# Kernel tuning notes

Measured on AMD Instinct MI355X. Metric: run time of the kernel, lower is better.

The kernel has to match this reference:

```python
import jax, jax.numpy as jnp
import numpy as np

E, NH, NL, NP = 256, 8, 4, 4
D = E // NH
SPATIAL_SHAPES = np.array([[100, 134], [50, 67], [25, 34], [13, 17]], dtype=np.int64)
B = 2


def setup_inputs() -> dict:
    key = jax.random.key(0)
    ks = jax.random.split(key, 12)
    Lin = int((SPATIAL_SHAPES[:, 0] * SPATIAL_SHAPES[:, 1]).sum())
    Lq = Lin
    s = 0.02
    return {
        'query': jax.random.normal(ks[0], (Lq, B, E), jnp.float32),
        'value': jax.random.normal(ks[1], (Lin, B, E), jnp.float32),
        'reference_points': jax.random.uniform(ks[2], (B, Lq, NL, 2), jnp.float32),
        'spatial_shapes': SPATIAL_SHAPES,
        'W_value': jax.random.normal(ks[3], (E, E), jnp.float32) * s,
        'b_value': jnp.zeros((E,), jnp.float32),
        'W_offset': jax.random.normal(ks[4], (E, NH * NL * NP * 2), jnp.float32) * s,
        'b_offset': jax.random.normal(ks[5], (NH * NL * NP * 2,), jnp.float32) * 0.5,
        'W_attn': jax.random.normal(ks[6], (E, NH * NL * NP), jnp.float32) * s,
        'b_attn': jnp.zeros((NH * NL * NP,), jnp.float32),
        'W_out': jax.random.normal(ks[7], (E, E), jnp.float32) * s,
        'b_out': jnp.zeros((E,), jnp.float32),
    }


def _ms_deform_attn(value, spatial_shapes, sampling_locations, attention_weights):
    # value: (B, Lin, NH, D); sampling_locations: (B, Lq, NH, NL, NP, 2) in [0,1]
    # attention_weights: (B, Lq, NH, NL, NP)
    b, _, nh, d = value.shape
    lq = sampling_locations.shape[1]
    npnt = sampling_locations.shape[4]
    shapes = np.asarray(spatial_shapes)
    out = jnp.zeros((b, nh, lq, d), value.dtype)
    start = 0
    for l in range(shapes.shape[0]):
        H, W = int(shapes[l, 0]), int(shapes[l, 1])
        vl = value[:, start:start + H * W].transpose(0, 2, 1, 3)  # (B, NH, H*W, D)
        loc = sampling_locations[:, :, :, l].transpose(0, 2, 1, 3, 4)  # (B, NH, Lq, P, 2)
        # grid_sample align_corners=False convention (matches CUDA kernel)
        x = loc[..., 0] * W - 0.5
        y = loc[..., 1] * H - 0.5
        x0 = jnp.floor(x)
        y0 = jnp.floor(y)
        dx = x - x0
        dy = y - y0
        x0i = x0.astype(jnp.int32)
        y0i = y0.astype(jnp.int32)
        acc = jnp.zeros((b, nh, lq, npnt, d), value.dtype)
        corners = [
            (x0i, y0i, (1.0 - dx) * (1.0 - dy)),
            (x0i + 1, y0i, dx * (1.0 - dy)),
            (x0i, y0i + 1, (1.0 - dx) * dy),
            (x0i + 1, y0i + 1, dx * dy),
        ]
        for xi, yi, w in corners:
            valid = ((xi >= 0) & (xi < W) & (yi >= 0) & (yi < H)).astype(value.dtype)
            idx = jnp.clip(yi, 0, W - 1 if False else H - 1) * 0  # placeholder removed below
            idx = jnp.clip(yi, 0, H - 1) * W + jnp.clip(xi, 0, W - 1)  # (B, NH, Lq, P)
            g = jnp.take_along_axis(vl, idx.reshape(b, nh, -1)[..., None], axis=2)
            g = g.reshape(b, nh, lq, npnt, d)
            acc = acc + g * (w * valid)[..., None]
        awl = attention_weights[:, :, :, l].transpose(0, 2, 1, 3)  # (B, NH, Lq, P)
        out = out + jnp.einsum('bhqpd,bhqp->bhqd', acc, awl)
        start += H * W
    return out.transpose(0, 2, 1, 3).reshape(b, lq, nh * d)  # (B, Lq, E)


def reference(query, value, reference_points, spatial_shapes,
              W_value, b_value, W_offset, b_offset, W_attn, b_attn, W_out, b_out):
    q = query.transpose(1, 0, 2)   # (B, Lq, E)
    v = value.transpose(1, 0, 2)   # (B, Lin, E)
    b, lq, _ = q.shape
    lin = v.shape[1]
    v = (v @ W_value + b_value).reshape(b, lin, NH, D)
    offsets = (q @ W_offset + b_offset).reshape(b, lq, NH, NL, NP, 2)
    attn = (q @ W_attn + b_attn).reshape(b, lq, NH, NL, NP)
    attn = jax.nn.softmax(attn, axis=-1)  # softmax over points (as in source)
    shapes_f = jnp.asarray(np.asarray(spatial_shapes), jnp.float32)
    offset_normalizer = jnp.stack([shapes_f[:, 1], shapes_f[:, 0]], -1)  # (NL, 2) = (w, h)
    loc = reference_points[:, :, None, :, None, :] + offsets / offset_normalizer[None, None, None, :, None, :]
    out = _ms_deform_attn(v, spatial_shapes, loc, attn)  # (B, Lq, E)
    out = out @ W_out + b_out
    return out.transpose(1, 0, 2)  # (Lq, B, E)
```

## Files before the change

kernel.cpp:

```cpp
#include <hip/hip_runtime.h>
#include <math.h>

#define LQ    17821
#define MROWS 35642
#define KD    256

typedef __attribute__((ext_vector_type(8))) short bf16x8;
typedef __attribute__((ext_vector_type(4))) float f32x4;

__device__ __forceinline__ short f2bf(float f) {
  union { float f; unsigned u; } c; c.f = f;
  unsigned u = c.u;
  return (short)((u + 0x7fffu + ((u >> 16) & 1u)) >> 16);
}
__device__ __forceinline__ float bf2f(short s) {
  union { unsigned u; float f; } c;
  c.u = ((unsigned)(unsigned short)s) << 16;
  return c.f;
}

__global__ __launch_bounds__(256) void wtrans_all(
    const float* __restrict__ Wv, const float* __restrict__ Woff,
    const float* __restrict__ Wat, const float* __restrict__ Wout,
    const float* __restrict__ boff, const float* __restrict__ bat,
    short* __restrict__ wT, float* __restrict__ fbias)
{
  int sel = blockIdx.y;
  int idx = blockIdx.x * 256 + threadIdx.x;
  if (sel == 4) {
    if (idx < 384) fbias[idx] = (idx < 256) ? boff[idx] : bat[idx - 256];
    return;
  }
  const float* W = sel == 0 ? Wv : sel == 1 ? Woff : sel == 2 ? Wat : Wout;
  short* Wt = wT + (sel == 0 ? 0 : sel == 1 ? 65536 : sel == 2 ? 131072 : 163840);
  int N = (sel == 2) ? 128 : 256;
  if (idx < N * 256) {
    int n = idx >> 8, k = idx & 255;
    Wt[idx] = f2bf(W[k * N + n]);
  }
}

template<bool A_F32, bool OUT_BF16>
__global__ __launch_bounds__(256) void gemm_bf16(
    const void* __restrict__ Araw, const short* __restrict__ Bt,
    const float* __restrict__ bias, void* __restrict__ Cout,
    int M, int N)
{
  __shared__ short As[128 * 40];
  __shared__ short Bs[128 * 40];

  const int tid = threadIdx.x;
  const int bm = blockIdx.x * 128;
  const int bn = blockIdx.y * 128;
  const int wave = tid >> 6;
  const int lane = tid & 63;
  const int wm = (wave & 1) * 64;
  const int wn = (wave >> 1) * 64;
  const int ln = lane & 15;
  const int lk = (lane >> 4) * 8;

  f32x4 acc[4][4];
#pragma unroll
  for (int i = 0; i < 4; ++i)
#pragma unroll
    for (int j = 0; j < 4; ++j) acc[i][j] = (f32x4){0.f, 0.f, 0.f, 0.f};

  const int r0 = tid >> 2,  s0 = (tid & 3) * 8;
  const int r1 = r0 + 64;
  const size_t arow0 = (size_t)min(bm + r0, M - 1) * KD;
  const size_t arow1 = (size_t)min(bm + r1, M - 1) * KD;
  const size_t brow0 = (size_t)(bn + r0) * KD;
  const size_t brow1 = (size_t)(bn + r1) * KD;

  const short* Ab = (const short*)Araw;
  const float* Af = (const float*)Araw;

  for (int k0 = 0; k0 < KD; k0 += 32) {
    bf16x8 a0, a1;
    if (A_F32) {
      float4 p0 = *(const float4*)(Af + arow0 + k0 + s0);
      float4 p1 = *(const float4*)(Af + arow0 + k0 + s0 + 4);
      float4 p2 = *(const float4*)(Af + arow1 + k0 + s0);
      float4 p3 = *(const float4*)(Af + arow1 + k0 + s0 + 4);
      a0[0] = f2bf(p0.x); a0[1] = f2bf(p0.y); a0[2] = f2bf(p0.z); a0[3] = f2bf(p0.w);
      a0[4] = f2bf(p1.x); a0[5] = f2bf(p1.y); a0[6] = f2bf(p1.z); a0[7] = f2bf(p1.w);
      a1[0] = f2bf(p2.x); a1[1] = f2bf(p2.y); a1[2] = f2bf(p2.z); a1[3] = f2bf(p2.w);
      a1[4] = f2bf(p3.x); a1[5] = f2bf(p3.y); a1[6] = f2bf(p3.z); a1[7] = f2bf(p3.w);
    } else {
      a0 = *(const bf16x8*)(Ab + arow0 + k0 + s0);
      a1 = *(const bf16x8*)(Ab + arow1 + k0 + s0);
    }
    bf16x8 b0 = *(const bf16x8*)(Bt + brow0 + k0 + s0);
    bf16x8 b1 = *(const bf16x8*)(Bt + brow1 + k0 + s0);
    __syncthreads();
    *(bf16x8*)&As[r0 * 40 + s0] = a0;
    *(bf16x8*)&As[r1 * 40 + s0] = a1;
    *(bf16x8*)&Bs[r0 * 40 + s0] = b0;
    *(bf16x8*)&Bs[r1 * 40 + s0] = b1;
    __syncthreads();

    bf16x8 af[4], bfr[4];
#pragma unroll
    for (int i = 0; i < 4; ++i)
      af[i] = *(const bf16x8*)&As[(wm + i * 16 + ln) * 40 + lk];
#pragma unroll
    for (int j = 0; j < 4; ++j)
      bfr[j] = *(const bf16x8*)&Bs[(wn + j * 16 + ln) * 40 + lk];
#pragma unroll
    for (int i = 0; i < 4; ++i)
#pragma unroll
      for (int j = 0; j < 4; ++j)
        acc[i][j] = __builtin_amdgcn_mfma_f32_16x16x32_bf16(af[i], bfr[j], acc[i][j], 0, 0, 0);
  }

#pragma unroll
  for (int j = 0; j < 4; ++j) {
    const int col = bn + wn + j * 16 + ln;
    const float bb = bias[col];
#pragma unroll
    for (int i = 0; i < 4; ++i) {
      const int row0 = bm + wm + i * 16 + (lane >> 4) * 4;
#pragma unroll
      for (int r = 0; r < 4; ++r) {
        const int row = row0 + r;
        if (row < M) {
          float v = acc[i][j][r] + bb;
          if (OUT_BF16)
            ((short*)Cout)[(size_t)row * N + col] = f2bf(v);
          else
            ((float*)Cout)[(size_t)row * N + col] = v;
        }
      }
    }
  }
}

__global__ __launch_bounds__(256) void msda_sample(
    const short* __restrict__ vproj, const float* __restrict__ oa,
    const float* __restrict__ refp, short* __restrict__ out)
{
  static constexpr int LVL_H[4] = {100, 50, 25, 13};
  static constexpr int LVL_W[4] = {134, 67, 34, 17};
  static constexpr int LVL_S[4] = {0, 13400, 16750, 17600};

  __shared__ int4   s_off[8 * 8 * 17];
  __shared__ float4 s_w[8 * 8 * 17];

  const int tid = threadIdx.x;
  const int m0 = blockIdx.x * 8;

#pragma unroll
  for (int it = 0; it < 4; ++it) {
    int w = tid + it * 256;
    int mr = w >> 7;
    int rest = w & 127;
    int h = rest >> 4;
    int lp = rest & 15;
    int l = lp >> 2;
    int p = lp & 3;
    int m = m0 + mr;
    if (m < MROWS) {
      int b = m & 1, q = m >> 1;
      const int Hl = LVL_H[l], Wl = LVL_W[l], Sl = LVL_S[l];
      const float fW = (float)Wl, fH = (float)Hl;

      float4 av = *(const float4*)(oa + (size_t)m * 384 + 256 + h * 16 + l * 4);
      float a0 = av.x, a1 = av.y, a2 = av.z, a3 = av.w;
      float mx = fmaxf(fmaxf(a0, a1), fmaxf(a2, a3));
      a0 = __expf(a0 - mx); a1 = __expf(a1 - mx);
      a2 = __expf(a2 - mx); a3 = __expf(a3 - mx);
      float sel = (p == 0) ? a0 : (p == 1) ? a1 : (p == 2) ? a2 : a3;
      float aw = sel / (a0 + a1 + a2 + a3);

      const float* oPtr = oa + (size_t)m * 384 + h * 32 + l * 8 + p * 2;
      float ox = oPtr[0], oy = oPtr[1];
      const float* rPtr = refp + ((size_t)b * LQ + q) * 8 + l * 2;
      float rx = rPtr[0], ry = rPtr[1];

      float x = (rx + ox / fW) * fW - 0.5f;
      float y = (ry + oy / fH) * fH - 0.5f;
      float x0f = floorf(x), y0f = floorf(y);
      float dx = x - x0f, dy = y - y0f;
      int x0 = (int)x0f, y0 = (int)y0f;
      int x1 = x0 + 1, y1 = y0 + 1;

      float w00 = (1.f - dx) * (1.f - dy) * aw;
      float w10 = dx * (1.f - dy) * aw;
      float w01 = (1.f - dx) * dy * aw;
      float w11 = dx * dy * aw;

      bool vx0 = (x0 >= 0) & (x0 < Wl);
      bool vx1 = (x1 >= 0) & (x1 < Wl);
      bool vy0 = (y0 >= 0) & (y0 < Hl);
      bool vy1 = (y1 >= 0) & (y1 < Hl);
      int cx0 = min(max(x0, 0), Wl - 1);
      int cx1 = min(max(x1, 0), Wl - 1);
      int cy0 = min(max(y0, 0), Hl - 1);
      int cy1 = min(max(y1, 0), Hl - 1);

      int r0 = Sl + cy0 * Wl;
      int r1 = Sl + cy1 * Wl;
      int e = (mr * 8 + h) * 17 + lp;
      s_off[e] = make_int4(((r0 + cx0) * 2 + b) << 8,
                           ((r0 + cx1) * 2 + b) << 8,
                           ((r1 + cx0) * 2 + b) << 8,
                           ((r1 + cx1) * 2 + b) << 8);
      s_w[e] = make_float4((vy0 & vx0) ? w00 : 0.f,
                           (vy0 & vx1) ? w10 : 0.f,
                           (vy1 & vx0) ? w01 : 0.f,
                           (vy1 & vx1) ? w11 : 0.f);
    }
  }
  __syncthreads();

  const int mr = tid >> 5;
  const int t = tid & 31;
  const int h = t >> 2;
  const int dq = t & 3;
  const int m = m0 + mr;
  if (m >= MROWS) return;

  const int laneOff = h * 32 + dq * 8;
  const int ebase = (mr * 8 + h) * 17;
  float acc[8];
#pragma unroll
  for (int e = 0; e < 8; ++e) acc[e] = 0.f;

#pragma unroll 4
  for (int lp = 0; lp < 16; ++lp) {
    int4 off = s_off[ebase + lp];
    float4 wv = s_w[ebase + lp];
    bf16x8 u00 = *(const bf16x8*)(vproj + off.x + laneOff);
    bf16x8 u10 = *(const bf16x8*)(vproj + off.y + laneOff);
    bf16x8 u01 = *(const bf16x8*)(vproj + off.z + laneOff);
    bf16x8 u11 = *(const bf16x8*)(vproj + off.w + laneOff);
#pragma unroll
    for (int e = 0; e < 8; ++e) {
      acc[e] = fmaf(wv.x, bf2f(u00[e]), acc[e]);
      acc[e] = fmaf(wv.y, bf2f(u10[e]), acc[e]);
      acc[e] = fmaf(wv.z, bf2f(u01[e]), acc[e]);
      acc[e] = fmaf(wv.w, bf2f(u11[e]), acc[e]);
    }
  }

  bf16x8 o;
#pragma unroll
  for (int e = 0; e < 8; ++e) o[e] = f2bf(acc[e]);
  *(bf16x8*)(out + (size_t)m * 256 + laneOff) = o;
}

extern "C" void kernel_launch(void* const* d_in, const int* in_sizes, int n_in,
                              void* d_out, int out_size, void* d_ws, size_t ws_size,
                              hipStream_t stream)
{
  const float* query = (const float*)d_in[0];
  const float* value = (const float*)d_in[1];
  const float* refp  = (const float*)d_in[2];
  const float* Wv   = (const float*)d_in[4];
  const float* bv   = (const float*)d_in[5];
  const float* Woff = (const float*)d_in[6];
  const float* boff = (const float*)d_in[7];
  const float* Wat  = (const float*)d_in[8];
  const float* bat  = (const float*)d_in[9];
  const float* Wout = (const float*)d_in[10];
  const float* bout = (const float*)d_in[11];
  float* out = (float*)d_out;

  const size_t NELT = (size_t)MROWS * 256;
  short* wT    = (short*)d_ws;
  float* fbias = (float*)(wT + 229376);
  short* vproj = (short*)(fbias + 384);
  short* accb  = vproj + NELT;
  float* oa    = (float*)(accb + NELT);

  dim3 blk(256, 1, 1);
  int gm = (MROWS + 127) / 128;

  wtrans_all<<<dim3(256, 5), blk, 0, stream>>>(Wv, Woff, Wat, Wout, boff, bat, wT, fbias);

  gemm_bf16<true,  true ><<<dim3(gm, 2), blk, 0, stream>>>(value, wT,         bv,    vproj, MROWS, 256);
  gemm_bf16<true,  false><<<dim3(gm, 3), blk, 0, stream>>>(query, wT + 65536, fbias, oa,    MROWS, 384);

  msda_sample<<<dim3((MROWS + 7) / 8), blk, 0, stream>>>(vproj, oa, refp, accb);

  gemm_bf16<false, false><<<dim3(gm, 2), blk, 0, stream>>>(accb, wT + 163840, bout, out, MROWS, 256);
}
```

Before: 302.6 us.

## Rewrite GEMM to stage full-K A tile in LDS and merge projection launches

Replaces the K-looped GEMM, which synchronised twice per 32-wide K step, with a kernel that loads the whole 128x256 A tile into XOR-swizzled LDS once. B fragments are read directly from global memory with double-buffered register prefetch. The value and query projections are merged into a single launch with 5 column blocks, and a launch_bounds occupancy hint of 2 is added. The cost is 64KB of LDS per block, which limits occupancy, and B reads that now bypass shared memory and rely on cache reuse.

Result: slower. 330.8 us (+9.3%).

```diff
diff --git a/kernel.cpp b/kernel.cpp
--- a/kernel.cpp
+++ b/kernel.cpp
@@ -40,24 +40,53 @@
   }
 }
 
-template<bool A_F32, bool OUT_BF16>
-__global__ __launch_bounds__(256) void gemm_bf16(
-    const void* __restrict__ Araw, const short* __restrict__ Bt,
-    const float* __restrict__ bias, void* __restrict__ Cout,
-    int M, int N)
+template<bool A_F32>
+__global__ __launch_bounds__(256, 2) void gemm_fullk(
+    const void* __restrict__ A0, const void* __restrict__ A1,
+    const short* __restrict__ Bt0, const short* __restrict__ Bt1,
+    const float* __restrict__ bias0, const float* __restrict__ bias1,
+    short* __restrict__ out0, float* __restrict__ out1,
+    int M, int N1, int gybase)
 {
-  __shared__ short As[128 * 40];
-  __shared__ short Bs[128 * 40];
+  __shared__ bf16x8 As[32 * 128];
 
   const int tid = threadIdx.x;
+  const int gy = blockIdx.y + gybase;
+  const bool sel0 = gy < 2;
+  const void* A = sel0 ? A0 : A1;
+  const short* Bt = sel0 ? Bt0 : Bt1;
+  const float* bias = sel0 ? bias0 : bias1;
+  const int bn = (sel0 ? gy : gy - 2) * 128;
   const int bm = blockIdx.x * 128;
-  const int bn = blockIdx.y * 128;
+
+  {
+    const int r = tid >> 1;
+    const int h2 = tid & 1;
+    const size_t arow = (size_t)min(bm + r, M - 1) * KD;
+#pragma unroll
+    for (int i = 0; i < 16; ++i) {
+      const int s = h2 * 16 + i;
+      bf16x8 v;
+      if (A_F32) {
+        const float* ap = (const float*)A + arow + s * 8;
+        float4 p0 = *(const float4*)ap;
+        float4 p1 = *(const float4*)(ap + 4);
+        v[0] = f2bf(p0.x); v[1] = f2bf(p0.y); v[2] = f2bf(p0.z); v[3] = f2bf(p0.w);
+        v[4] = f2bf(p1.x); v[5] = f2bf(p1.y); v[6] = f2bf(p1.z); v[7] = f2bf(p1.w);
+      } else {
+        v = *(const bf16x8*)((const short*)A + arow + s * 8);
+      }
+      As[s * 128 + (r ^ (s & 7))] = v;
+    }
+  }
+  __syncthreads();
+
+  const int lane = tid & 63;
   const int wave = tid >> 6;
-  const int lane = tid & 63;
   const int wm = (wave & 1) * 64;
   const int wn = (wave >> 1) * 64;
   const int ln = lane & 15;
-  const int lk = (lane >> 4) * 8;
+  const int lq = lane >> 4;
 
   f32x4 acc[4][4];
 #pragma unroll
@@ -65,70 +94,59 @@
 #pragma unroll
     for (int j = 0; j < 4; ++j) acc[i][j] = (f32x4){0.f, 0.f, 0.f, 0.f};
 
-  const int r0 = tid >> 2,  s0 = (tid & 3) * 8;
-  const int r1 = r0 + 64;
-  const size_t arow0 = (size_t)min(bm + r0, M - 1) * KD;
-  const size_t arow1 = (size_t)min(bm + r1, M - 1) * KD;
-  const size_t brow0 = (size_t)(bn + r0) * KD;
-  const size_t brow1 = (size_t)(bn + r1) * KD;
-
-  const short* Ab = (const short*)Araw;
-  const float* Af = (const float*)Araw;
-
-  for (int k0 = 0; k0 < KD; k0 += 32) {
-    bf16x8 a0, a1;
-    if (A_F32) {
-      float4 p0 = *(const float4*)(Af + arow0 + k0 + s0);
-      float4 p1 = *(const float4*)(Af + arow0 + k0 + s0 + 4);
-      float4 p2 = *(const float4*)(Af + arow1 + k0 + s0);
-      float4 p3 = *(const float4*)(Af + arow1 + k0 + s0 + 4);
-      a0[0] = f2bf(p0.x); a0[1] = f2bf(p0.y); a0[2] = f2bf(p0.z); a0[3] = f2bf(p0.w);
-      a0[4] = f2bf(p1.x); a0[5] = f2bf(p1.y); a0[6] = f2bf(p1.z); a0[7] = f2bf(p1.w);
-      a1[0] = f2bf(p2.x); a1[1] = f2bf(p2.y); a1[2] = f2bf(p2.z); a1[3] = f2bf(p2.w);
-      a1[4] = f2bf(p3.x); a1[5] = f2bf(p3.y); a1[6] = f2bf(p3.z); a1[7] = f2bf(p3.w);
-    } else {
-      a0 = *(const bf16x8*)(Ab + arow0 + k0 + s0);
-      a1 = *(const bf16x8*)(Ab + arow1 + k0 + s0);
-    }
-    bf16x8 b0 = *(const bf16x8*)(Bt + brow0 + k0 + s0);
-    bf16x8 b1 = *(const bf16x8*)(Bt + brow1 + k0 + s0);
-    __syncthreads();
-    *(bf16x8*)&As[r0 * 40 + s0] = a0;
-    *(bf16x8*)&As[r1 * 40 + s0] = a1;
-    *(bf16x8*)&Bs[r0 * 40 + s0] = b0;
-    *(bf16x8*)&Bs[r1 * 40 + s0] = b1;
-    __syncthreads();
-
-    bf16x8 af[4], bfr[4];
+  bf16x8 af[2][4], bf[2][4];
+
+#define LD_A(kk, dst)                                                        \
+  {                                                                          \
+    const int sA = (kk) * 4 + lq;                                            \
+    const int swz = sA & 7;                                                  \
+    _Pragma("unroll")                                                        \
+    for (int i = 0; i < 4; ++i)                                              \
+      dst[i] = As[sA * 128 + ((wm + i * 16 + ln) ^ swz)];                    \
+  }
+#define LD_B(kk, dst)                                                        \
+  {                                                                          \
+    _Pragma("unroll")                                                        \
+    for (int j = 0; j < 4; ++j)                                              \
+      dst[j] = *(const bf16x8*)(Bt + (size_t)(bn + wn + j * 16 + ln) * KD +  \
+                                (kk) * 32 + lq * 8);                         \
+  }
+
+  LD_A(0, af[0]);
+  LD_B(0, bf[0]);
+#pragma unroll
+  for (int kk = 0; kk < 8; ++kk) {
+    const int cur = kk & 1, nxt = cur ^ 1;
+    if (kk < 7) {
+      LD_B(kk + 1, bf[nxt]);
+      LD_A(kk + 1, af[nxt]);
+    }
 #pragma unroll
     for (int i = 0; i < 4; ++i)
-      af[i] = *(const bf16x8*)&As[(wm + i * 16 + ln) * 40 + lk];
-#pragma unroll
-    for (int j = 0; j < 4; ++j)
-      bfr[j] = *(const bf16x8*)&Bs[(wn + j * 16 + ln) * 40 + lk];
-#pragma unroll
-    for (int i = 0; i < 4; ++i)
 #pragma unroll
       for (int j = 0; j < 4; ++j)
-        acc[i][j] = __builtin_amdgcn_mfma_f32_16x16x32_bf16(af[i], bfr[j], acc[i][j], 0, 0, 0);
-  }
-
+        acc[i][j] = __builtin_amdgcn_mfma_f32_16x16x32_bf16(af[cur][i], bf[cur][j], acc[i][j], 0, 0, 0);
+  }
+#undef LD_A
+#undef LD_B
+
+  const int N = sel0 ? 256 : N1;
 #pragma unroll
   for (int j = 0; j < 4; ++j) {
     const int col = bn + wn + j * 16 + ln;
     const float bb = bias[col];
 #pragma unroll
     for (int i = 0; i < 4; ++i) {
-      const int row0 = bm + wm + i * 16 + (lane >> 4) * 4;
+      const int row0 = bm + wm + i * 16 + lq * 4;
 #pragma unroll
       for (int r = 0; r < 4; ++r) {
         const int row = row0 + r;
         if (row < M) {
           float v = acc[i][j][r] + bb;
-          if (OUT_BF16)
-            ((short*)Cout)[(size_t)row * N + col] = f2bf(v);
+          if (sel0)
+            out0[(size_t)row * 256 + col] = f2bf(v);
           else
-            ((float*)Cout)[(size_t)row * N + col] = v;
+            out1[(size_t)row * N + col] = v;
         }
       }
     }
@@ -278,10 +296,11 @@
 
   wtrans_all<<<dim3(256, 5), blk, 0, stream>>>(Wv, Woff, Wat, Wout, boff, bat, wT, fbias);
 
-  gemm_bf16<true,  true ><<<dim3(gm, 2), blk, 0, stream>>>(value, wT,         bv,    vproj, MROWS, 256);
-  gemm_bf16<true,  false><<<dim3(gm, 3), blk, 0, stream>>>(query, wT + 65536, fbias, oa,    MROWS, 384);
+  gemm_fullk<true><<<dim3(gm, 5), blk, 0, stream>>>(
+      value, query, wT, wT + 65536, bv, fbias, vproj, oa, MROWS, 384, 0);
 
   msda_sample<<<dim3((MROWS + 7) / 8), blk, 0, stream>>>(vproj, oa, refp, accb);
 
-  gemm_bf16<false, false><<<dim3(gm, 2), blk, 0, stream>>>(accb, wT + 163840, bout, out, MROWS, 256);
-}
+  gemm_fullk<false><<<dim3(gm, 2), blk, 0, stream>>>(
+      accb, accb, wT + 163840, wT + 163840, bout, bout, nullptr, out, MROWS, 256, 2);
+}
```
